# Performance work log

Measured on AMD Instinct MI355X. Metric: run time of the kernel, lower is better.

## Reference

```python
import jax, jax.numpy as jnp
import numpy as np

EPS = 1e-08


def setup_inputs() -> dict:
    key = jax.random.key(0)
    k1, k2 = jax.random.split(key)
    query_features = jax.random.normal(k1, (64, 1024, 32, 32), dtype=jnp.float32)
    support_features = jax.random.normal(k2, (25, 1024, 32, 32), dtype=jnp.float32)
    return {"query_features": query_features, "support_features": support_features}


def reference(query_features, support_features):
    B, C, h, w = support_features.shape
    NQ = query_features.shape[0]
    # Covariance over channels: flatten support to (C, B*h*w), center, GEMM.
    support = jnp.transpose(support_features, (1, 0, 2, 3)).reshape(C, -1)
    centered = support - jnp.mean(support, axis=1, keepdims=True)
    N = B * h * w
    cov = (centered @ centered.T) / (N - 1 + EPS)  # (C, C)
    # Queries: (NQ, C, d), L2-normalize each channel row over spatial dim.
    q = query_features.reshape(NQ, C, -1)
    q = q / (jnp.linalg.norm(q, axis=2, keepdims=True) + EPS)
    # diag(q^T cov q) without materializing (d, d): cov@q then elementwise reduce over C.
    cq = jnp.einsum('cD,nDd->ncd', cov, q)  # (NQ, C, d)
    scores = jnp.mean(jnp.sum(q * cq, axis=1), axis=1)  # (NQ,)
    return scores
```

## Files before the change

### kernel.cpp

```cpp
#include <hip/hip_runtime.h>

#define NQ   64
#define CCH  1024
#define DSP  1024
#define NSUP 25600
#define KSLICES 8
#define NK_COV 50

typedef __attribute__((ext_vector_type(4))) float f32x4;
typedef __attribute__((ext_vector_type(8))) __bf16 bf16x8;

#define WAITVM(N) asm volatile("s_waitcnt vmcnt(" #N ")" ::: "memory")
#define WAITLGKM0() asm volatile("s_waitcnt lgkmcnt(0)" ::: "memory")
#define BAR() __builtin_amdgcn_s_barrier()

__device__ inline unsigned short f2bf(float x) {
  unsigned u = __builtin_bit_cast(unsigned, x);
  u += 0x7fffu + ((u >> 16) & 1u);
  return (unsigned short)(u >> 16);
}

__global__ __launch_bounds__(256) void zero_kernel(float4* __restrict__ cov4,
                                                   float4* __restrict__ out4) {
  const int i = blockIdx.x * 256 + threadIdx.x;
  cov4[i] = make_float4(0.f, 0.f, 0.f, 0.f);
  if (i < 16) out4[i] = make_float4(0.f, 0.f, 0.f, 0.f);
}


__global__ __launch_bounds__(256) void mean_center_kernel(
    const float* __restrict__ sup, float* __restrict__ mean,
    unsigned short* __restrict__ Sb, int write_sb) {
  const int c = blockIdx.x;
  const int tid = threadIdx.x;
  float s = 0.f;
  for (int qd = tid; qd < 6400; qd += 256) {
    const int b = qd >> 8, s4 = (qd & 255) << 2;
    const float4 v = *(const float4*)(sup + ((size_t)b * CCH + c) * DSP + s4);
    s += v.x + v.y + v.z + v.w;
  }
  __shared__ float red[256];
  red[tid] = s;
  __syncthreads();
  for (int st = 128; st > 0; st >>= 1) {
    if (tid < st) red[tid] += red[tid + st];
    __syncthreads();
  }
  const float m = red[0] * (1.0f / 25600.0f);
  if (tid == 0) mean[c] = m;
  if (write_sb) {
    for (int qd = tid; qd < 6400; qd += 256) {
      const int b = qd >> 8, s4 = (qd & 255) << 2;
      const float4 v = *(const float4*)(sup + ((size_t)b * CCH + c) * DSP + s4);
      ushort4 o;
      o.x = f2bf(v.x - m); o.y = f2bf(v.y - m);
      o.z = f2bf(v.z - m); o.w = f2bf(v.w - m);
      *(ushort4*)(Sb + (size_t)c * NSUP + b * DSP + s4) = o;
    }
  }
}

__global__ __launch_bounds__(256) void qnorm_kernel(
    const float* __restrict__ q, float* __restrict__ qfac,
    unsigned short* __restrict__ Qb, int write_qb) {
  const int row = blockIdx.x * 4 + (threadIdx.x >> 6);
  const int l = threadIdx.x & 63;
  const float4* src = (const float4*)(q + (size_t)row * DSP);
  float4 v[4];
  float ss = 0.f;
#pragma unroll
  for (int i = 0; i < 4; ++i) {
    v[i] = src[l + 64 * i];
    ss += v[i].x * v[i].x + v[i].y * v[i].y + v[i].z * v[i].z + v[i].w * v[i].w;
  }
#pragma unroll
  for (int off = 32; off > 0; off >>= 1) ss += __shfl_xor(ss, off);
  const float f = 1.0f / (sqrtf(ss) + 1e-8f);
  if (l == 0) qfac[row] = f;
  if (write_qb) {
#pragma unroll
    for (int i = 0; i < 4; ++i) {
      ushort4 o;
      o.x = f2bf(v[i].x * f); o.y = f2bf(v[i].y * f);
      o.z = f2bf(v[i].z * f); o.w = f2bf(v[i].w * f);
      *(ushort4*)(Qb + (size_t)row * DSP + (size_t)(l + 64 * i) * 4) = o;
    }
  }
}


__device__ inline void stage_glds(const unsigned short* __restrict__ src, int ld,
                                  int row0, int k0, unsigned short* lds) {
  const int tid = threadIdx.x;
  const int w = tid >> 6;
#pragma unroll
  for (int it = 0; it < 4; ++it) {
    const int ci = it * 256 + tid;
    const int r = ci >> 3;
    const int kc = ((ci & 7) ^ (r & 7)) << 3;
    const unsigned short* g = src + (size_t)(row0 + r) * ld + k0 + kc;
    unsigned short* lb = lds + ((it * 256 + w * 64) << 3);
    __builtin_amdgcn_global_load_lds((const __attribute__((address_space(1))) void*)g,
                                     (__attribute__((address_space(3))) void*)lb,
                                     16, 0, 0);
  }
}

__device__ inline void stage_sup_f32(const float* __restrict__ sup,
                                     const float* __restrict__ mean,
                                     int row0, int k0, unsigned short* lds) {
  const int tid = threadIdx.x;
#pragma unroll
  for (int it = 0; it < 4; ++it) {
    const int ci = it * 256 + tid;
    const int r = ci >> 3, kc = (ci & 7) << 3;
    const int c = row0 + r;
    const int k = k0 + kc;
    const int b = k >> 10, sp = k & 1023;
    const float4* g = (const float4*)(sup + ((size_t)b * CCH + c) * DSP + sp);
    const float4 v0 = g[0], v1 = g[1];
    const float m = mean[c];
    union { unsigned short h[8]; int4 q; } pk;
    pk.h[0] = f2bf(v0.x - m); pk.h[1] = f2bf(v0.y - m);
    pk.h[2] = f2bf(v0.z - m); pk.h[3] = f2bf(v0.w - m);
    pk.h[4] = f2bf(v1.x - m); pk.h[5] = f2bf(v1.y - m);
    pk.h[6] = f2bf(v1.z - m); pk.h[7] = f2bf(v1.w - m);
    *(int4*)(lds + (size_t)(r * 8 + ((ci & 7) ^ (r & 7))) * 8) = pk.q;
  }
}

__device__ inline void stage_q_f32(const float* __restrict__ qn,
                                   const float* __restrict__ qfacn,
                                   int row0, int k0, unsigned short* lds) {
  const int tid = threadIdx.x;
#pragma unroll
  for (int it = 0; it < 4; ++it) {
    const int ci = it * 256 + tid;
    const int r = ci >> 3, kc = (ci & 7) << 3;
    const int c = row0 + r;
    const float4* g = (const float4*)(qn + (size_t)c * DSP + k0 + kc);
    const float4 v0 = g[0], v1 = g[1];
    const float f = qfacn[c];
    union { unsigned short h[8]; int4 q; } pk;
    pk.h[0] = f2bf(v0.x * f); pk.h[1] = f2bf(v0.y * f);
    pk.h[2] = f2bf(v0.z * f); pk.h[3] = f2bf(v0.w * f);
    pk.h[4] = f2bf(v1.x * f); pk.h[5] = f2bf(v1.y * f);
    pk.h[6] = f2bf(v1.z * f); pk.h[7] = f2bf(v1.w * f);
    *(int4*)(lds + (size_t)(r * 8 + ((ci & 7) ^ (r & 7))) * 8) = pk.q;
  }
}

__device__ inline void compute_step(const unsigned short* lA, const unsigned short* lB,
                                    int wr, int wc, int lr, int kg, f32x4 acc[4][4]) {
  const int sc = (lr & 7) << 3;
  __builtin_amdgcn_s_setprio(1);
#pragma unroll
  for (int kk = 0; kk < 64; kk += 32) {
    const int col = (kk + kg) ^ sc;
    bf16x8 a[4], b[4];
#pragma unroll
    for (int i = 0; i < 4; ++i)
      a[i] = *(const bf16x8*)(const void*)(lA + (wr + i * 16 + lr) * 64 + col);
#pragma unroll
    for (int j = 0; j < 4; ++j)
      b[j] = *(const bf16x8*)(const void*)(lB + (wc + j * 16 + lr) * 64 + col);
#pragma unroll
    for (int i = 0; i < 4; ++i)
#pragma unroll
      for (int j = 0; j < 4; ++j)
        acc[i][j] = __builtin_amdgcn_mfma_f32_16x16x32_bf16(a[i], b[j], acc[i][j], 0, 0, 0);
  }
  __builtin_amdgcn_s_setprio(0);
}

__device__ inline void pre_compute_sync_nondiag() {
  WAITVM(8); BAR(); __builtin_amdgcn_sched_barrier(0);
}
__device__ inline void pre_compute_sync_diag() {
  WAITVM(4); BAR(); __builtin_amdgcn_sched_barrier(0);
}
__device__ inline void pre_compute_sync_last() {
  WAITVM(0); BAR(); __builtin_amdgcn_sched_barrier(0);
}
__device__ inline void post_compute_sync() {
  WAITLGKM0(); BAR(); __builtin_amdgcn_sched_barrier(0);
}

__device__ inline void decode_tile(int t, int& ti, int& tj) {
  int rem = t; ti = 0;
  while (rem >= 8 - ti) { rem -= 8 - ti; ++ti; }
  tj = ti + rem;
}

template <bool F32>
__global__ __launch_bounds__(256) void cov_kernel(
    const unsigned short* __restrict__ Sb, const float* __restrict__ sup,
    const float* __restrict__ mean, float* __restrict__ cov) {
  __shared__ unsigned short lA[2][128 * 64];
  __shared__ unsigned short lB[2][128 * 64];
  const int wg = blockIdx.x;
  const int ks = wg & 7;
  int ti, tj; decode_tile(wg >> 3, ti, tj);
  const bool diag = (ti == tj);
  const int tid = threadIdx.x, l = tid & 63, w = tid >> 6;
  const int wr = (w >> 1) * 64, wc = (w & 1) * 64, lr = l & 15, kg = (l >> 4) * 8;
  f32x4 acc[4][4];
#pragma unroll
  for (int i = 0; i < 4; ++i)
#pragma unroll
    for (int j = 0; j < 4; ++j) acc[i][j] = 0.f;

  const int kbase = ks * (NSUP / KSLICES);

  if (F32) {
    stage_sup_f32(sup, mean, ti * 128, kbase, lA[0]);
    if (!diag) stage_sup_f32(sup, mean, tj * 128, kbase, lB[0]);
    __syncthreads();
    int cur = 0;
    for (int kt = 0; kt < NK_COV; ++kt) {
      if (kt + 1 < NK_COV) {
        const int k1 = kbase + (kt + 1) * 64;
        stage_sup_f32(sup, mean, ti * 128, k1, lA[cur ^ 1]);
        if (!diag) stage_sup_f32(sup, mean, tj * 128, k1, lB[cur ^ 1]);
      }
      compute_step(lA[cur], diag ? lA[cur] : lB[cur], wr, wc, lr, kg, acc);
      __syncthreads();
      cur ^= 1;
    }
  } else {
    stage_glds(Sb, NSUP, ti * 128, kbase, lA[0]);
    if (!diag) stage_glds(Sb, NSUP, tj * 128, kbase, lB[0]);
    int cur = 0;
    for (int kt = 0; kt < NK_COV; ++kt) {
      if (kt + 1 < NK_COV) {
        const int k1 = kbase + (kt + 1) * 64;
        stage_glds(Sb, NSUP, ti * 128, k1, lA[cur ^ 1]);
        if (!diag) {
          stage_glds(Sb, NSUP, tj * 128, k1, lB[cur ^ 1]);
          pre_compute_sync_nondiag();
        } else {
          pre_compute_sync_diag();
        }
      } else {
        pre_compute_sync_last();
      }
      compute_step(lA[cur], diag ? lA[cur] : lB[cur], wr, wc, lr, kg, acc);
      post_compute_sync();
      cur ^= 1;
    }
  }

  const float scale = 1.0f / (25599.0f + 1e-8f);
  const int rbase = ti * 128 + wr + (l >> 4) * 4;
  const int cbase = tj * 128 + wc + (l & 15);
#pragma unroll
  for (int i = 0; i < 4; ++i)
#pragma unroll
    for (int j = 0; j < 4; ++j)
#pragma unroll
      for (int r = 0; r < 4; ++r)
        atomicAdd(&cov[(size_t)(rbase + i * 16 + r) * CCH + cbase + j * 16],
                  acc[i][j][r] * scale);
}

template <bool F32>
__global__ __launch_bounds__(256) void gram_kernel(
    const unsigned short* __restrict__ Qb, const float* __restrict__ q,
    const float* __restrict__ qfac, const float* __restrict__ cov,
    float* __restrict__ out) {
  __shared__ unsigned short lA[2][128 * 64];
  __shared__ unsigned short lB[2][128 * 64];
  const int wg = blockIdx.x;
  const int xcd = wg & 7, slot = wg >> 3;
  const int n = xcd * 8 + slot / 36;
  int ti, tj; decode_tile(slot % 36, ti, tj);
  const bool diag = (ti == tj);
  const int tid = threadIdx.x, l = tid & 63, w = tid >> 6;
  const int wr = (w >> 1) * 64, wc = (w & 1) * 64, lr = l & 15, kg = (l >> 4) * 8;
  f32x4 acc[4][4];
#pragma unroll
  for (int i = 0; i < 4; ++i)
#pragma unroll
    for (int j = 0; j < 4; ++j) acc[i][j] = 0.f;

  const float* qn = q + (size_t)n * CCH * DSP;
  const float* qfacn = qfac + (size_t)n * CCH;

  stage_q_f32(qn, qfacn, ti * 128, 0, lA[0]);
  if (!diag) stage_q_f32(qn, qfacn, tj * 128, 0, lB[0]);
  __syncthreads();
  int cur = 0;
  for (int kt = 0; kt < 16; ++kt) {
    if (kt + 1 < 16) {
      const int k1 = (kt + 1) * 64;
      stage_q_f32(qn, qfacn, ti * 128, k1, lA[cur ^ 1]);
      if (!diag) stage_q_f32(qn, qfacn, tj * 128, k1, lB[cur ^ 1]);
    }
    compute_step(lA[cur], diag ? lA[cur] : lB[cur], wr, wc, lr, kg, acc);
    __syncthreads();
    cur ^= 1;
  }

  float s = 0.f;
  const int rbase = ti * 128 + wr + (l >> 4) * 4;
  const int cbase = tj * 128 + wc + (l & 15);
#pragma unroll
  for (int i = 0; i < 4; ++i)
#pragma unroll
    for (int j = 0; j < 4; ++j)
#pragma unroll
      for (int r = 0; r < 4; ++r)
        s += acc[i][j][r] * cov[(size_t)(rbase + i * 16 + r) * CCH + cbase + j * 16];
  if (!diag) s *= 2.0f;
  s *= (1.0f / 1024.0f);
#pragma unroll
  for (int off = 32; off > 0; off >>= 1) s += __shfl_xor(s, off);
  if (l == 0) atomicAdd(&out[n], s);
}


__device__ inline void stage256(const unsigned short* __restrict__ src,
                                int row0, int k0, unsigned short* lds_base) {
  const int tid = threadIdx.x;
  const int wid = tid >> 6;
#pragma unroll
  for (int it = 0; it < 4; ++it) {
    const int ci = it * 512 + tid;
    const int r = ci >> 3;
    const int kc = ((ci & 7) ^ (r & 7)) << 3;
    const unsigned short* g = src + (size_t)(row0 + r) * DSP + k0 + kc;
    unsigned short* lb = lds_base + ((it * 512 + (wid << 6)) << 3);
    __builtin_amdgcn_global_load_lds((const __attribute__((address_space(1))) void*)g,
                                     (__attribute__((address_space(3))) void*)lb,
                                     16, 0, 0);
  }
}

__device__ inline void rd_a4(const unsigned short* A, int q, int col, int lr, bf16x8 a[4]) {
#pragma unroll
  for (int i = 0; i < 4; ++i)
    a[i] = *(const bf16x8*)(const void*)(A + (q * 64 + i * 16 + lr) * 64 + col);
}
__device__ inline void rd_b4(const unsigned short* B, int brow, int col, int lr, bf16x8 b[4]) {
#pragma unroll
  for (int j = 0; j < 4; ++j)
    b[j] = *(const bf16x8*)(const void*)(B + (brow + j * 16 + lr) * 64 + col);
}
__device__ inline void mfma16(const bf16x8 a[4], const bf16x8 b[4], f32x4 (*acc)[4]) {
  __builtin_amdgcn_s_setprio(1);
#pragma unroll
  for (int i = 0; i < 4; ++i)
#pragma unroll
    for (int j = 0; j < 4; ++j)
      acc[i][j] = __builtin_amdgcn_mfma_f32_16x16x32_bf16(a[i], b[j], acc[i][j], 0, 0, 0);
  __builtin_amdgcn_s_setprio(0);
}

__global__ __launch_bounds__(512, 2) void gram256_kernel(
    const unsigned short* __restrict__ Qb, const float* __restrict__ cov,
    float* __restrict__ out) {
  __shared__ unsigned short lds[65536];
  const int wg = blockIdx.x;
  const int xcd = wg & 7, slot = wg >> 3;
  const int n = xcd * 8 + slot / 10;
  int rem = slot % 10, ti = 0;
  while (rem >= 4 - ti) { rem -= 4 - ti; ++ti; }
  const int tj = ti + rem;
  const int tid = threadIdx.x, l = tid & 63, wid = tid >> 6;
  const int wm = wid >> 2, wn = wid & 3;
  const int lr = l & 15, kg = (l >> 4) * 8;
  const int sw = (lr & 7) << 3;
  const unsigned short* Qn = Qb + (size_t)n * CCH * DSP;

  f32x4 acc[8][4];
#pragma unroll
  for (int i = 0; i < 8; ++i)
#pragma unroll
    for (int j = 0; j < 4; ++j) acc[i][j] = 0.f;

  stage256(Qn, ti * 256, 0, lds);
  stage256(Qn, tj * 256, 0, lds + 16384);
  WAITVM(0);
  BAR();

  for (int t = 0; t < 16; ++t) {
    const int cb = (t & 1) << 15;
    if (t < 15) {
      const int nb = cb ^ 32768;
      stage256(Qn, ti * 256, (t + 1) * 64, lds + nb);
      stage256(Qn, tj * 256, (t + 1) * 64, lds + nb + 16384);
    }
    const unsigned short* A = lds + cb + wm * 8192;
    const unsigned short* B = lds + cb + 16384 + (wn >> 1) * 8192;
    const int brow = (wn & 1) * 64;
    bf16x8 a[4], b[4];
#pragma unroll
    for (int kk = 0; kk < 64; kk += 32) {
      const int col = (kk + kg) ^ sw;
      rd_b4(B, brow, col, lr, b);
      rd_a4(A, 0, col, lr, a);
      BAR();
      mfma16(a, b, &acc[0]);
      BAR();
      rd_a4(A, 1, col, lr, a);
      BAR();
      mfma16(a, b, &acc[4]);
      if (kk == 32 && t < 15) WAITVM(0);
      BAR();
    }
  }

  float s = 0.f;
  const int rbase = ti * 256 + wm * 128 + (l >> 4) * 4;
  const int cbase = tj * 256 + wn * 64 + (l & 15);
#pragma unroll
  for (int i = 0; i < 8; ++i)
#pragma unroll
    for (int j = 0; j < 4; ++j)
#pragma unroll
      for (int r = 0; r < 4; ++r)
        s += acc[i][j][r] * cov[(size_t)(rbase + i * 16 + r) * CCH + cbase + j * 16];
  if (ti != tj) s *= 2.0f;
  s *= (1.0f / 1024.0f);
#pragma unroll
  for (int off = 32; off > 0; off >>= 1) s += __shfl_xor(s, off);
  if (l == 0) atomicAdd(&out[n], s);
}

extern "C" void kernel_launch(void* const* d_in, const int* in_sizes, int n_in,
                              void* d_out, int out_size, void* d_ws, size_t ws_size,
                              hipStream_t stream) {
  const float* q = (const float*)d_in[0];
  const float* sup = (const float*)d_in[1];
  float* out = (float*)d_out;

  char* ws = (char*)d_ws;
  float* mean = (float*)ws;
  float* qfac = (float*)(ws + (4 << 10));
  float* cov  = (float*)(ws + (4 << 10) + (256 << 10));
  unsigned short* Sb = (unsigned short*)(ws + (4 << 10) + (256 << 10) + (4 << 20));
  unsigned short* Qb = Sb + (size_t)CCH * NSUP;
  const size_t need_fat = (size_t)(4 << 10) + (256 << 10) + (4 << 20) +
                          (size_t)CCH * NSUP * 2 + (size_t)NQ * CCH * DSP * 2;
  const bool fat = ws_size >= need_fat;

  zero_kernel<<<1024, 256, 0, stream>>>((float4*)cov, (float4*)out);

  mean_center_kernel<<<CCH, 256, 0, stream>>>(sup, mean, Sb, fat ? 1 : 0);
  qnorm_kernel<<<NQ * CCH / 4, 256, 0, stream>>>(q, qfac, Qb, fat ? 1 : 0);

  if (fat) {
    cov_kernel<false><<<dim3(288), 256, 0, stream>>>(Sb, sup, mean, cov);
    gram256_kernel<<<dim3(640), 512, 0, stream>>>(Qb, cov, out);
  } else {
    cov_kernel<true><<<dim3(288), 256, 0, stream>>>(Sb, sup, mean, cov);
    gram_kernel<true><<<dim3(8 * 8 * 36), 256, 0, stream>>>(Qb, q, qfac, cov, out);
  }
}
```

Before: 301.9 us.

## Deepen prefetch pipelines in cov and gram kernels, cache support row in LDS

```diff
diff --git a/kernel.cpp b/kernel.cpp
--- a/kernel.cpp
+++ b/kernel.cpp
@@ -13,6 +13,7 @@
 #define WAITVM(N) asm volatile("s_waitcnt vmcnt(" #N ")" ::: "memory")
 #define WAITLGKM0() asm volatile("s_waitcnt lgkmcnt(0)" ::: "memory")
 #define BAR() __builtin_amdgcn_s_barrier()
+#define SCHED0() __builtin_amdgcn_sched_barrier(0)
 
 __device__ inline unsigned short f2bf(float x) {
   unsigned u = __builtin_bit_cast(unsigned, x);
@@ -28,30 +29,32 @@
 }
 
 
-__global__ __launch_bounds__(256) void mean_center_kernel(
+__global__ __launch_bounds__(512) void mean_center_kernel(
     const float* __restrict__ sup, float* __restrict__ mean,
     unsigned short* __restrict__ Sb, int write_sb) {
+  __shared__ float4 row[6400];
+  __shared__ float red[512];
   const int c = blockIdx.x;
   const int tid = threadIdx.x;
   float s = 0.f;
-  for (int qd = tid; qd < 6400; qd += 256) {
+  for (int qd = tid; qd < 6400; qd += 512) {
     const int b = qd >> 8, s4 = (qd & 255) << 2;
     const float4 v = *(const float4*)(sup + ((size_t)b * CCH + c) * DSP + s4);
+    row[qd] = v;
     s += v.x + v.y + v.z + v.w;
   }
-  __shared__ float red[256];
   red[tid] = s;
   __syncthreads();
-  for (int st = 128; st > 0; st >>= 1) {
+  for (int st = 256; st > 0; st >>= 1) {
     if (tid < st) red[tid] += red[tid + st];
     __syncthreads();
   }
   const float m = red[0] * (1.0f / 25600.0f);
   if (tid == 0) mean[c] = m;
   if (write_sb) {
-    for (int qd = tid; qd < 6400; qd += 256) {
+    for (int qd = tid; qd < 6400; qd += 512) {
+      const float4 v = row[qd];
       const int b = qd >> 8, s4 = (qd & 255) << 2;
-      const float4 v = *(const float4*)(sup + ((size_t)b * CCH + c) * DSP + s4);
       ushort4 o;
       o.x = f2bf(v.x - m); o.y = f2bf(v.y - m);
       o.z = f2bf(v.z - m); o.w = f2bf(v.w - m);
@@ -104,6 +107,38 @@
                                      (__attribute__((address_space(3))) void*)lb,
                                      16, 0, 0);
   }
+}
+
+__device__ inline void stage256(const unsigned short* __restrict__ src,
+                                int row0, int k0, unsigned short* lds_base) {
+  const int tid = threadIdx.x;
+  const int wid = tid >> 6;
+#pragma unroll
+  for (int it = 0; it < 4; ++it) {
+    const int ci = it * 512 + tid;
+    const int r = ci >> 3;
+    const int kc = ((ci & 7) ^ (r & 7)) << 3;
+    const unsigned short* g = src + (size_t)(row0 + r) * DSP + k0 + kc;
+    unsigned short* lb = lds_base + ((it * 512 + (wid << 6)) << 3);
+    __builtin_amdgcn_global_load_lds((const __attribute__((address_space(1))) void*)g,
+                                     (__attribute__((address_space(3))) void*)lb,
+                                     16, 0, 0);
+  }
+}
+
+__device__ inline void rd4(const unsigned short* base, int r0, int col, int lr, bf16x8 f[4]) {
+#pragma unroll
+  for (int i = 0; i < 4; ++i)
+    f[i] = *(const bf16x8*)(const void*)(base + (r0 + i * 16 + lr) * 64 + col);
+}
+__device__ inline void mfma16(const bf16x8 a[4], const bf16x8 b[4], f32x4 (*acc)[4]) {
+  __builtin_amdgcn_s_setprio(1);
+#pragma unroll
+  for (int i = 0; i < 4; ++i)
+#pragma unroll
+    for (int j = 0; j < 4; ++j)
+      acc[i][j] = __builtin_amdgcn_mfma_f32_16x16x32_bf16(a[i], b[j], acc[i][j], 0, 0, 0);
+  __builtin_amdgcn_s_setprio(0);
 }
 
 __device__ inline void stage_sup_f32(const float* __restrict__ sup,
@@ -128,7 +163,6 @@
     *(int4*)(lds + (size_t)(r * 8 + ((ci & 7) ^ (r & 7))) * 8) = pk.q;
   }
 }
-
 __device__ inline void stage_q_f32(const float* __restrict__ qn,
                                    const float* __restrict__ qfacn,
                                    int row0, int k0, unsigned short* lds) {
@@ -149,41 +183,21 @@
     *(int4*)(lds + (size_t)(r * 8 + ((ci & 7) ^ (r & 7))) * 8) = pk.q;
   }
 }
-
 __device__ inline void compute_step(const unsigned short* lA, const unsigned short* lB,
                                     int wr, int wc, int lr, int kg, f32x4 acc[4][4]) {
   const int sc = (lr & 7) << 3;
-  __builtin_amdgcn_s_setprio(1);
 #pragma unroll
   for (int kk = 0; kk < 64; kk += 32) {
     const int col = (kk + kg) ^ sc;
     bf16x8 a[4], b[4];
+    rd4(lA, wr, col, lr, a);
+    rd4(lB, wc, col, lr, b);
+    mfma16(a, b, (f32x4(*)[4])acc);
 #pragma unroll
     for (int i = 0; i < 4; ++i)
-      a[i] = *(const bf16x8*)(const void*)(lA + (wr + i * 16 + lr) * 64 + col);
-#pragma unroll
-    for (int j = 0; j < 4; ++j)
-      b[j] = *(const bf16x8*)(const void*)(lB + (wc + j * 16 + lr) * 64 + col);
-#pragma unroll
-    for (int i = 0; i < 4; ++i)
-#pragma unroll
-      for (int j = 0; j < 4; ++j)
-        acc[i][j] = __builtin_amdgcn_mfma_f32_16x16x32_bf16(a[i], b[j], acc[i][j], 0, 0, 0);
-  }
-  __builtin_amdgcn_s_setprio(0);
-}
-
-__device__ inline void pre_compute_sync_nondiag() {
-  WAITVM(8); BAR(); __builtin_amdgcn_sched_barrier(0);
-}
-__device__ inline void pre_compute_sync_diag() {
-  WAITVM(4); BAR(); __builtin_amdgcn_sched_barrier(0);
-}
-__device__ inline void pre_compute_sync_last() {
-  WAITVM(0); BAR(); __builtin_amdgcn_sched_barrier(0);
-}
-__device__ inline void post_compute_sync() {
-  WAITLGKM0(); BAR(); __builtin_amdgcn_sched_barrier(0);
+#pragma unroll
+      for (int j = 0; j < 4; ++j) (void)0;
+  }
 }
 
 __device__ inline void decode_tile(int t, int& ti, int& tj) {
@@ -196,14 +210,14 @@
 __global__ __launch_bounds__(256) void cov_kernel(
     const unsigned short* __restrict__ Sb, const float* __restrict__ sup,
     const float* __restrict__ mean, float* __restrict__ cov) {
-  __shared__ unsigned short lA[2][128 * 64];
-  __shared__ unsigned short lB[2][128 * 64];
+  __shared__ unsigned short clds[32768];
   const int wg = blockIdx.x;
   const int ks = wg & 7;
   int ti, tj; decode_tile(wg >> 3, ti, tj);
   const bool diag = (ti == tj);
   const int tid = threadIdx.x, l = tid & 63, w = tid >> 6;
   const int wr = (w >> 1) * 64, wc = (w & 1) * 64, lr = l & 15, kg = (l >> 4) * 8;
+  const int sw = (lr & 7) << 3;
   f32x4 acc[4][4];
 #pragma unroll
   for (int i = 0; i < 4; ++i)
@@ -213,40 +227,53 @@
   const int kbase = ks * (NSUP / KSLICES);
 
   if (F32) {
-    stage_sup_f32(sup, mean, ti * 128, kbase, lA[0]);
-    if (!diag) stage_sup_f32(sup, mean, tj * 128, kbase, lB[0]);
+    unsigned short* lA0 = clds;
+    stage_sup_f32(sup, mean, ti * 128, kbase, lA0);
+    if (!diag) stage_sup_f32(sup, mean, tj * 128, kbase, lA0 + 8192);
     __syncthreads();
-    int cur = 0;
     for (int kt = 0; kt < NK_COV; ++kt) {
+      const int cb = (kt & 1) * 16384;
+      const int nb = cb ^ 16384;
       if (kt + 1 < NK_COV) {
         const int k1 = kbase + (kt + 1) * 64;
-        stage_sup_f32(sup, mean, ti * 128, k1, lA[cur ^ 1]);
-        if (!diag) stage_sup_f32(sup, mean, tj * 128, k1, lB[cur ^ 1]);
+        stage_sup_f32(sup, mean, ti * 128, k1, clds + nb);
+        if (!diag) stage_sup_f32(sup, mean, tj * 128, k1, clds + nb + 8192);
       }
-      compute_step(lA[cur], diag ? lA[cur] : lB[cur], wr, wc, lr, kg, acc);
+      compute_step(clds + cb, diag ? clds + cb : clds + cb + 8192, wr, wc, lr, kg, acc);
       __syncthreads();
-      cur ^= 1;
     }
   } else {
-    stage_glds(Sb, NSUP, ti * 128, kbase, lA[0]);
-    if (!diag) stage_glds(Sb, NSUP, tj * 128, kbase, lB[0]);
-    int cur = 0;
-    for (int kt = 0; kt < NK_COV; ++kt) {
-      if (kt + 1 < NK_COV) {
-        const int k1 = kbase + (kt + 1) * 64;
-        stage_glds(Sb, NSUP, ti * 128, k1, lA[cur ^ 1]);
-        if (!diag) {
-          stage_glds(Sb, NSUP, tj * 128, k1, lB[cur ^ 1]);
-          pre_compute_sync_nondiag();
-        } else {
-          pre_compute_sync_diag();
+    stage_glds(Sb, NSUP, ti * 128, kbase, clds);
+    if (!diag) stage_glds(Sb, NSUP, tj * 128, kbase, clds + 8192);
+    stage_glds(Sb, NSUP, ti * 128, kbase + 64, clds + 16384);
+    if (!diag) stage_glds(Sb, NSUP, tj * 128, kbase + 64, clds + 16384 + 8192);
+    for (int t = 0; t < NK_COV; ++t) {
+      const int cb = (t & 1) * 16384;
+      if (t < NK_COV - 1) { if (diag) { WAITVM(4); } else { WAITVM(8); } }
+      else { WAITVM(0); }
+      BAR(); SCHED0();
+      const unsigned short* A = clds + cb;
+      const unsigned short* B = diag ? A : A + 8192;
+      bf16x8 a[4], b[4];
+      {
+        const int col = kg ^ sw;
+        rd4(A, wr, col, lr, a);
+        rd4(B, wc, col, lr, b);
+        mfma16(a, b, (f32x4(*)[4])acc);
+      }
+      {
+        const int col = (32 + kg) ^ sw;
+        rd4(A, wr, col, lr, a);
+        rd4(B, wc, col, lr, b);
+        WAITLGKM0();
+        BAR(); SCHED0();
+        if (t + 2 < NK_COV) {
+          const int k2 = kbase + (t + 2) * 64;
+          stage_glds(Sb, NSUP, ti * 128, k2, clds + cb);
+          if (!diag) stage_glds(Sb, NSUP, tj * 128, k2, clds + cb + 8192);
         }
-      } else {
-        pre_compute_sync_last();
+        mfma16(a, b, (f32x4(*)[4])acc);
       }
-      compute_step(lA[cur], diag ? lA[cur] : lB[cur], wr, wc, lr, kg, acc);
-      post_compute_sync();
-      cur ^= 1;
     }
   }
 
@@ -263,11 +290,9 @@
                   acc[i][j][r] * scale);
 }
 
-template <bool F32>
-__global__ __launch_bounds__(256) void gram_kernel(
-    const unsigned short* __restrict__ Qb, const float* __restrict__ q,
-    const float* __restrict__ qfac, const float* __restrict__ cov,
-    float* __restrict__ out) {
+__global__ __launch_bounds__(256) void gram_kernel_f32(
+    const float* __restrict__ q, const float* __restrict__ qfac,
+    const float* __restrict__ cov, float* __restrict__ out) {
   __shared__ unsigned short lA[2][128 * 64];
   __shared__ unsigned short lB[2][128 * 64];
   const int wg = blockIdx.x;
@@ -318,44 +343,6 @@
   if (l == 0) atomicAdd(&out[n], s);
 }
 
-
-__device__ inline void stage256(const unsigned short* __restrict__ src,
-                                int row0, int k0, unsigned short* lds_base) {
-  const int tid = threadIdx.x;
-  const int wid = tid >> 6;
-#pragma unroll
-  for (int it = 0; it < 4; ++it) {
-    const int ci = it * 512 + tid;
-    const int r = ci >> 3;
-    const int kc = ((ci & 7) ^ (r & 7)) << 3;
-    const unsigned short* g = src + (size_t)(row0 + r) * DSP + k0 + kc;
-    unsigned short* lb = lds_base + ((it * 512 + (wid << 6)) << 3);
-    __builtin_amdgcn_global_load_lds((const __attribute__((address_space(1))) void*)g,
-                                     (__attribute__((address_space(3))) void*)lb,
-                                     16, 0, 0);
-  }
-}
-
-__device__ inline void rd_a4(const unsigned short* A, int q, int col, int lr, bf16x8 a[4]) {
-#pragma unroll
-  for (int i = 0; i < 4; ++i)
-    a[i] = *(const bf16x8*)(const void*)(A + (q * 64 + i * 16 + lr) * 64 + col);
-}
-__device__ inline void rd_b4(const unsigned short* B, int brow, int col, int lr, bf16x8 b[4]) {
-#pragma unroll
-  for (int j = 0; j < 4; ++j)
-    b[j] = *(const bf16x8*)(const void*)(B + (brow + j * 16 + lr) * 64 + col);
-}
-__device__ inline void mfma16(const bf16x8 a[4], const bf16x8 b[4], f32x4 (*acc)[4]) {
-  __builtin_amdgcn_s_setprio(1);
-#pragma unroll
-  for (int i = 0; i < 4; ++i)
-#pragma unroll
-    for (int j = 0; j < 4; ++j)
-      acc[i][j] = __builtin_amdgcn_mfma_f32_16x16x32_bf16(a[i], b[j], acc[i][j], 0, 0, 0);
-  __builtin_amdgcn_s_setprio(0);
-}
-
 __global__ __launch_bounds__(512, 2) void gram256_kernel(
     const unsigned short* __restrict__ Qb, const float* __restrict__ cov,
     float* __restrict__ out) {
@@ -366,6 +353,7 @@
   int rem = slot % 10, ti = 0;
   while (rem >= 4 - ti) { rem -= 4 - ti; ++ti; }
   const int tj = ti + rem;
+  const bool diag = (ti == tj);
   const int tid = threadIdx.x, l = tid & 63, wid = tid >> 6;
   const int wm = wid >> 2, wn = wid & 3;
   const int lr = l & 15, kg = (l >> 4) * 8;
@@ -379,34 +367,40 @@
     for (int j = 0; j < 4; ++j) acc[i][j] = 0.f;
 
   stage256(Qn, ti * 256, 0, lds);
-  stage256(Qn, tj * 256, 0, lds + 16384);
-  WAITVM(0);
-  BAR();
+  if (!diag) stage256(Qn, tj * 256, 0, lds + 16384);
+  stage256(Qn, ti * 256, 64, lds + 32768);
+  if (!diag) stage256(Qn, tj * 256, 64, lds + 32768 + 16384);
 
   for (int t = 0; t < 16; ++t) {
     const int cb = (t & 1) << 15;
-    if (t < 15) {
-      const int nb = cb ^ 32768;
-      stage256(Qn, ti * 256, (t + 1) * 64, lds + nb);
-      stage256(Qn, tj * 256, (t + 1) * 64, lds + nb + 16384);
-    }
+    if (t < 15) { if (diag) { WAITVM(4); } else { WAITVM(8); } }
+    else { WAITVM(0); }
+    BAR(); SCHED0();
     const unsigned short* A = lds + cb + wm * 8192;
-    const unsigned short* B = lds + cb + 16384 + (wn >> 1) * 8192;
+    const unsigned short* B = lds + cb + (diag ? 0 : 16384) + (wn >> 1) * 8192;
     const int brow = (wn & 1) * 64;
     bf16x8 a[4], b[4];
-#pragma unroll
-    for (int kk = 0; kk < 64; kk += 32) {
-      const int col = (kk + kg) ^ sw;
-      rd_b4(B, brow, col, lr, b);
-      rd_a4(A, 0, col, lr, a);
-      BAR();
+    {
+      const int col = kg ^ sw;
+      rd4(B, brow, col, lr, b);
+      rd4(A, 0, col, lr, a);
       mfma16(a, b, &acc[0]);
-      BAR();
-      rd_a4(A, 1, col, lr, a);
-      BAR();
+      rd4(A, 64, col, lr, a);
       mfma16(a, b, &acc[4]);
-      if (kk == 32 && t < 15) WAITVM(0);
-      BAR();
+    }
+    {
+      const int col = (32 + kg) ^ sw;
+      rd4(B, brow, col, lr, b);
+      rd4(A, 0, col, lr, a);
+      mfma16(a, b, &acc[0]);
+      rd4(A, 64, col, lr, a);
+      WAITLGKM0();
+      BAR(); SCHED0();
+      if (t + 2 < 16) {
+        stage256(Qn, ti * 256, (t + 2) * 64, lds + cb);
+        if (!diag) stage256(Qn, tj * 256, (t + 2) * 64, lds + cb + 16384);
+      }
+      mfma16(a, b, &acc[4]);
     }
   }
 
@@ -420,7 +414,7 @@
 #pragma unroll
       for (int r = 0; r < 4; ++r)
         s += acc[i][j][r] * cov[(size_t)(rbase + i * 16 + r) * CCH + cbase + j * 16];
-  if (ti != tj) s *= 2.0f;
+  if (!diag) s *= 2.0f;
   s *= (1.0f / 1024.0f);
 #pragma unroll
   for (int off = 32; off > 0; off >>= 1) s += __shfl_xor(s, off);
@@ -446,7 +440,7 @@
 
   zero_kernel<<<1024, 256, 0, stream>>>((float4*)cov, (float4*)out);
 
-  mean_center_kernel<<<CCH, 256, 0, stream>>>(sup, mean, Sb, fat ? 1 : 0);
+  mean_center_kernel<<<CCH, 512, 0, stream>>>(sup, mean, Sb, fat ? 1 : 0);
   qnorm_kernel<<<NQ * CCH / 4, 256, 0, stream>>>(q, qfac, Qb, fat ? 1 : 0);
 
   if (fat) {
@@ -454,6 +448,6 @@
     gram256_kernel<<<dim3(640), 512, 0, stream>>>(Qb, cov, out);
   } else {
     cov_kernel<true><<<dim3(288), 256, 0, stream>>>(Sb, sup, mean, cov);
-    gram_kernel<true><<<dim3(8 * 8 * 36), 256, 0, stream>>>(Qb, q, qfac, cov, out);
-  }
-}
+    gram_kernel_f32<<<dim3(8 * 8 * 36), 256, 0, stream>>>(q, qfac, cov, out);
+  }
+}
```

Result: faster. 270.4 us (-10.4%).
